# Kernel tuning notes

Measured on AMD Instinct MI355X. Metric: run time of the kernel, lower is better.

## Reference

```python
import jax, jax.numpy as jnp
import numpy as np

D = 256; H = 4; HD = 64; WBAND = 64; KLOC = 8; EMAK = 256
SUMDECAY = 0.9; STATEDECAY = 0.9; STEP = 0.5


def _dwconv(x, kern, pad):
    # x: (B,T,D), kern: (D,1,K) cross-correlation taps, causal left pad
    lhs = jnp.transpose(x, (0, 2, 1))
    out = jax.lax.conv_general_dilated(
        lhs, kern, (1,), [(pad, 0)],
        dimension_numbers=('NCH', 'OIH', 'NCH'),
        feature_group_count=x.shape[-1])
    return jnp.transpose(out, (0, 2, 1))


def _ln(x, g, b):
    m = jnp.mean(x, -1, keepdims=True)
    v = jnp.var(x, -1, keepdims=True)
    return (x - m) * jax.lax.rsqrt(v + 1e-5) * g + b


def _lin(x, w, b):
    return jnp.dot(x, w.T) + b


def _forward(parallel_repr, sequential_state, trajectory_summary, conv_w, conv_b,
             qkv_w, qkv_b, mo_w, mo_b, fg_w, fg_b, gkv_w, gkv_b, go_w, go_b,
             comb_w, comb_b, ffn1_w, ffn1_b, ffn2_w, ffn2_b, tr1_w, tr1_b,
             tr2_w, tr2_b, p2s_w, p2s_b, s2p_w, s2p_b,
             ln1_g, ln1_b, ln2_g, ln2_b, ln3_g, ln3_b, ln4_g, ln4_b):
    B, T, _ = parallel_repr.shape
    # Tier 1: local depthwise causal conv (window 8); torch pads both sides then slices [:T] == causal left pad
    local_history = _dwconv(parallel_repr, conv_w, KLOC - 1) + conv_b
    # Tier 2: banded causal attention (keep j in [i-63, i])
    qkv = _lin(parallel_repr, qkv_w, qkv_b).reshape(B, T, 3, H, HD)
    qkv = jnp.transpose(qkv, (2, 0, 3, 1, 4))  # (3,B,H,T,HD)
    q, k, v = qkv[0], qkv[1], qkv[2]
    idx = jnp.arange(T)
    band = (idx[:, None] >= idx[None, :]) & (idx[None, :] > idx[:, None] - WBAND)
    scores = jnp.einsum('bhqd,bhkd->bhqk', q, k) / jnp.sqrt(jnp.float32(HD))
    attn = jax.nn.softmax(jnp.where(band, scores, -1e9), -1)
    med = jnp.einsum('bhqk,bhkd->bhqd', attn, v)
    med = jnp.transpose(med, (0, 2, 1, 3)).reshape(B, T, D)
    med = _lin(med, mo_w, mo_b)
    fg = jax.nn.sigmoid(_lin(jnp.concatenate([parallel_repr, med], -1), fg_w, fg_b))
    medium_out = med * fg
    # Tier 3: causal cumulative (linear-attention style) global concepts
    gkv = _lin(parallel_repr, gkv_w, gkv_b)
    gk, gv = jnp.split(gkv, 2, -1)
    gk = jax.nn.elu(gk) + 1.0
    concepts = jnp.cumsum(gk * gv, 1) / (jnp.cumsum(gk, 1) + 1e-5)
    global_out = _lin(concepts, go_w, go_b)
    combined = _lin(jnp.concatenate([local_history, medium_out, global_out], -1), comb_w, comb_b)
    pr = _ln(parallel_repr + combined, ln1_g, ln1_b)
    # EMA summary via 256-tap causal depthwise conv: w[i] = (1-d)*d^i
    kE = min(T, EMAK)
    taps = (1.0 - SUMDECAY) * SUMDECAY ** jnp.arange(kE, dtype=jnp.float32)
    kern = jnp.broadcast_to(taps[::-1][None, None, :], (D, 1, kE))
    global_summary = _dwconv(pr, kern, kE - 1)
    guidance = _lin(pr, p2s_w, p2s_b)
    cs = jnp.concatenate([pr + 0.3 * guidance, global_summary], -1)
    deltas = jnp.tanh(_lin(jax.nn.gelu(_lin(cs, tr1_w, tr1_b), approximate=False), tr2_w, tr2_b))
    scaled = deltas * STEP
    # state accumulation via conv trick: acc[t] = sum_i d^i * delta[t-i]
    staps = STATEDECAY ** jnp.arange(kE, dtype=jnp.float32)
    skern = jnp.broadcast_to(staps[::-1][None, None, :], (D, 1, kE))
    acc = _dwconv(scaled, skern, kE - 1)
    dpow = STATEDECAY ** jnp.arange(1, T + 1, dtype=jnp.float32)
    pre_ln = sequential_state[:, None, :] * dpow[None, :, None] + acc
    states = _ln(pre_ln, ln3_g, ln3_b)
    seq_g = _lin(states, s2p_w, s2p_b)
    ffn = _lin(jax.nn.gelu(_lin(pr + 0.3 * seq_g, ffn1_w, ffn1_b), approximate=False), ffn2_w, ffn2_b)
    pr_out = _ln(pr + ffn, ln2_g, ln2_b)
    final_state = _ln(states[:, -1, :], ln4_g, ln4_b)
    final_traj = global_summary[:, -1, :]
    return pr_out, final_state, final_traj


def setup_inputs():
    key = jax.random.key(0)
    ks = jax.random.split(key, 20)
    B, T = 4, 2048
    s = 0.02
    def w(i, shape):
        return jax.random.normal(ks[i], shape, jnp.float32) * s
    return {
        'parallel_repr': jax.random.normal(ks[0], (B, T, D), jnp.float32),
        'sequential_state': jax.random.normal(ks[1], (B, D), jnp.float32),
        'trajectory_summary': jax.random.normal(ks[2], (B, D), jnp.float32),
        'conv_w': w(3, (D, 1, KLOC)), 'conv_b': jnp.zeros((D,)),
        'qkv_w': w(4, (3 * D, D)), 'qkv_b': jnp.zeros((3 * D,)),
        'mo_w': w(5, (D, D)), 'mo_b': jnp.zeros((D,)),
        'fg_w': w(6, (D, 2 * D)), 'fg_b': jnp.zeros((D,)),
        'gkv_w': w(7, (2 * D, D)), 'gkv_b': jnp.zeros((2 * D,)),
        'go_w': w(8, (D, D)), 'go_b': jnp.zeros((D,)),
        'comb_w': w(9, (D, 3 * D)), 'comb_b': jnp.zeros((D,)),
        'ffn1_w': w(10, (4 * D, D)), 'ffn1_b': jnp.zeros((4 * D,)),
        'ffn2_w': w(11, (D, 4 * D)), 'ffn2_b': jnp.zeros((D,)),
        'tr1_w': w(12, (2 * D, 2 * D)), 'tr1_b': jnp.zeros((2 * D,)),
        'tr2_w': w(13, (D, 2 * D)), 'tr2_b': jnp.zeros((D,)),
        'p2s_w': w(14, (D, D)), 'p2s_b': jnp.zeros((D,)),
        's2p_w': w(15, (D, D)), 's2p_b': jnp.zeros((D,)),
        'ln1_g': jnp.ones((D,)), 'ln1_b': jnp.zeros((D,)),
        'ln2_g': jnp.ones((D,)), 'ln2_b': jnp.zeros((D,)),
        'ln3_g': jnp.ones((D,)), 'ln3_b': jnp.zeros((D,)),
        'ln4_g': jnp.ones((D,)), 'ln4_b': jnp.zeros((D,)),
    }


def reference(parallel_repr, sequential_state, trajectory_summary, conv_w, conv_b,
              qkv_w, qkv_b, mo_w, mo_b, fg_w, fg_b, gkv_w, gkv_b, go_w, go_b,
              comb_w, comb_b, ffn1_w, ffn1_b, ffn2_w, ffn2_b, tr1_w, tr1_b,
              tr2_w, tr2_b, p2s_w, p2s_b, s2p_w, s2p_b,
              ln1_g, ln1_b, ln2_g, ln2_b, ln3_g, ln3_b, ln4_g, ln4_b):
    return _forward(parallel_repr, sequential_state, trajectory_summary, conv_w, conv_b,
                    qkv_w, qkv_b, mo_w, mo_b, fg_w, fg_b, gkv_w, gkv_b, go_w, go_b,
                    comb_w, comb_b, ffn1_w, ffn1_b, ffn2_w, ffn2_b, tr1_w, tr1_b,
                    tr2_w, tr2_b, p2s_w, p2s_b, s2p_w, s2p_b,
                    ln1_g, ln1_b, ln2_g, ln2_b, ln3_g, ln3_b, ln4_g, ln4_b)
```

## Files before the change

kernel.cpp:

```cpp
#include <hip/hip_runtime.h>
#include <hip/hip_bf16.h>
#include <math.h>

#define D_  256
#define T_  2048
#define B_  4
#define M_  (B_*T_)
#define H_  4
#define HD_ 64

#define NC_ 64
#define LCH (T_/NC_)

enum { OP_NONE=0, OP_SIGMUL=1, OP_ADDAUX=2, OP_AXPBY=3, OP_GELU=4, OP_TANHHALF=5 };

typedef short short8 __attribute__((ext_vector_type(8)));
typedef float f32x4  __attribute__((ext_vector_type(4)));

__device__ __forceinline__ float gelu_f(float x){ return 0.5f*x*(1.0f+erff(x*0.70710678118654752f)); }
__device__ __forceinline__ float sigmoid_f(float x){ return 1.0f/(1.0f+expf(-x)); }

__device__ __forceinline__ unsigned pk2(float a, float b){
    __hip_bfloat162 h = __float22bfloat162_rn(make_float2(a,b));
    union { __hip_bfloat162 h; unsigned u; } c; c.h = h; return c.u;
}

__global__ __launch_bounds__(256) void gemm_k(
    const float* __restrict__ A0, const float* __restrict__ W0, int ldw0, int K0,
    const float* __restrict__ A1, const float* __restrict__ W1, int ldw1, int K1,
    const float* __restrict__ A2, const float* __restrict__ W2, int ldw2, int K2,
    const float* __restrict__ bias, const float* __restrict__ aux,
    float* __restrict__ C, int ldc, int op, int ncol, float* __restrict__ vt)
{
    __shared__ unsigned short As[64*64];
    __shared__ unsigned short Ws[64*64];

    const int q8   = gridDim.x >> 3;
    const int lid  = (blockIdx.x & 7)*q8 + (blockIdx.x >> 3);
    const int brow = lid / ncol;
    const int bcol = lid - brow*ncol;
    const int row0 = brow*64, col0 = bcol*64;

    const int tid  = threadIdx.x;
    const int lane = tid & 63, wid = tid >> 6;
    const int wm = (wid >> 1)*32, wn = (wid & 1)*32;
    const int l15 = lane & 15, l4 = lane >> 4;
    const int srow = tid >> 3;
    const int sc8  = (tid & 7) * 8;

    f32x4 acc[2][2];
    #pragma unroll
    for (int i=0;i<2;++i)
        #pragma unroll
        for (int j=0;j<2;++j) acc[i][j] = (f32x4){0.f,0.f,0.f,0.f};

    float4 ra0,ra1,ra2,ra3, rw0,rw1,rw2,rw3;

    auto loadtile = [&](const float* A, const float* W, int ldw, int K, int kb){
        const float* ga = A + (size_t)(row0+srow)*K + kb + sc8;
        const float* ga2 = ga + (size_t)32*K;
        const float* gw = W + (size_t)(col0+srow)*ldw + kb + sc8;
        const float* gw2 = gw + (size_t)32*ldw;
        ra0 = *(const float4*)ga;  ra1 = *(const float4*)(ga+4);
        ra2 = *(const float4*)ga2; ra3 = *(const float4*)(ga2+4);
        rw0 = *(const float4*)gw;  rw1 = *(const float4*)(gw+4);
        rw2 = *(const float4*)gw2; rw3 = *(const float4*)(gw2+4);
    };
    auto storetile = [&](){
        const int i0 = (srow*64 + sc8) ^ ((srow&7)<<3);
        *(uint4*)&As[i0] = (uint4){pk2(ra0.x,ra0.y),pk2(ra0.z,ra0.w),pk2(ra1.x,ra1.y),pk2(ra1.z,ra1.w)};
        *(uint4*)&Ws[i0] = (uint4){pk2(rw0.x,rw0.y),pk2(rw0.z,rw0.w),pk2(rw1.x,rw1.y),pk2(rw1.z,rw1.w)};
        const int r2 = srow + 32;
        const int i1 = (r2*64 + sc8) ^ ((r2&7)<<3);
        *(uint4*)&As[i1] = (uint4){pk2(ra2.x,ra2.y),pk2(ra2.z,ra2.w),pk2(ra3.x,ra3.y),pk2(ra3.z,ra3.w)};
        *(uint4*)&Ws[i1] = (uint4){pk2(rw2.x,rw2.y),pk2(rw2.z,rw2.w),pk2(rw3.x,rw3.y),pk2(rw3.z,rw3.w)};
    };
    auto mfma_tile = [&](){
        #pragma unroll
        for (int ks=0;ks<2;++ks){
            const int koff = ks*32 + l4*8;
            short8 af[2], bf[2];
            #pragma unroll
            for (int f=0;f<2;++f){
                const int ar = wm + f*16 + l15;
                af[f] = *(const short8*)&As[(ar*64 + koff) ^ ((ar&7)<<3)];
                const int brn = wn + f*16 + l15;
                bf[f] = *(const short8*)&Ws[(brn*64 + koff) ^ ((brn&7)<<3)];
            }
            #pragma unroll
            for (int fm=0;fm<2;++fm)
                #pragma unroll
                for (int fn=0;fn<2;++fn)
                    acc[fm][fn] = __builtin_amdgcn_mfma_f32_16x16x32_bf16(
                        af[fm], bf[fn], acc[fm][fn], 0, 0, 0);
        }
    };

    const float* Ac = A0; const float* Wc = W0; int ldwc = ldw0, Kc = K0, kb = 0;
    loadtile(Ac, Wc, ldwc, Kc, 0);
    while (true){
        __syncthreads();
        storetile();
        __syncthreads();
        int nkb = kb + 64;
        const float* nA = Ac; const float* nW = Wc; int nld = ldwc, nK = Kc;
        bool have_next = true;
        if (nkb >= Kc){
            if (Ac == A0 && A1){ nA = A1; nW = W1; nld = ldw1; nK = K1; nkb = 0; }
            else if (Ac == A1 && A2){ nA = A2; nW = W2; nld = ldw2; nK = K2; nkb = 0; }
            else have_next = false;
        }
        if (have_next) loadtile(nA, nW, nld, nK, nkb);
        mfma_tile();
        if (!have_next) break;
        Ac = nA; Wc = nW; ldwc = nld; Kc = nK; kb = nkb;
    }

    #pragma unroll
    for (int fn=0;fn<2;++fn){
        const int n = col0 + wn + fn*16 + l15;
        const float bv = bias[n];
        const bool vwr = (vt != nullptr) && (n >= 512) && (n < 768);
        #pragma unroll
        for (int fm=0;fm<2;++fm){
            #pragma unroll
            for (int j=0;j<4;++j){
                const int m = row0 + wm + fm*16 + l4*4 + j;
                float v = acc[fm][fn][j] + bv;
                if (op==OP_GELU)          v = gelu_f(v);
                else if (op==OP_TANHHALF) v = 0.5f*tanhf(v);
                else if (op==OP_SIGMUL)   v = aux[(size_t)m*D_ + n]*sigmoid_f(v);
                else if (op==OP_ADDAUX)   v = v + aux[(size_t)m*D_ + n];
                else if (op==OP_AXPBY)    v = aux[(size_t)m*D_ + n] + 0.3f*v;
                C[(size_t)m*ldc + n] = v;
                if (vwr){
                    const int hh = (n-512)>>6, dd = (n-512)&63;
                    const int bb = m >> 11, tt = m & (T_-1);
                    vt[(((size_t)(bb*H_ + hh))*64 + dd)*T_ + tt] = v;
                }
            }
        }
    }
}

__global__ __launch_bounds__(256) void conv_k(const float* __restrict__ X,
    const float* __restrict__ w, const float* __restrict__ bias, float* __restrict__ out)
{
    int idx = blockIdx.x*256 + threadIdx.x;
    int d = idx & (D_-1);
    int bt = idx >> 8;
    int t = bt & (T_-1);
    float acc = bias[d];
    const float* xp = X + (size_t)bt*D_ + d;
    const float* wp = w + d*8;
    #pragma unroll
    for (int j=0;j<8;++j){
        int tt = t - 7 + j;
        if (tt >= 0) acc += xp[(size_t)(j-7)*D_] * wp[j];
    }
    out[idx] = acc;
}

__global__ __launch_bounds__(256) void attn_k(const float* __restrict__ QKVG,
    const float* __restrict__ VT, float* __restrict__ MED)
{
    __shared__ unsigned short Kl[128*64];
    __shared__ unsigned short Ql[64*64];
    __shared__ unsigned short Vl[64*128];
    const int b = blockIdx.z, h = blockIdx.y;
    const int t0 = blockIdx.x * 64;
    const int kb0 = t0 - 64;
    const int tid = threadIdx.x;

    {
        const int r0 = tid >> 3, c8 = (tid & 7) * 8;
        #pragma unroll
        for (int rep=0;rep<4;++rep){
            const int r = r0 + rep*32;
            const int kg = kb0 + r;
            uint4 pk = {0,0,0,0};
            if (kg >= 0){
                const float* gp = QKVG + ((size_t)(b*T_ + kg))*1280 + 256 + h*HD_ + c8;
                float4 x0 = *(const float4*)gp, x1 = *(const float4*)(gp+4);
                pk = (uint4){pk2(x0.x,x0.y),pk2(x0.z,x0.w),pk2(x1.x,x1.y),pk2(x1.z,x1.w)};
            }
            *(uint4*)&Kl[(r*64 + c8) ^ ((r&7)<<3)] = pk;
        }
        #pragma unroll
        for (int rep=0;rep<2;++rep){
            const int r = r0 + rep*32;
            const float* gp = QKVG + ((size_t)(b*T_ + t0 + r))*1280 + h*HD_ + c8;
            float4 x0 = *(const float4*)gp, x1 = *(const float4*)(gp+4);
            uint4 pq = (uint4){pk2(x0.x,x0.y),pk2(x0.z,x0.w),pk2(x1.x,x1.y),pk2(x1.z,x1.w)};
            *(uint4*)&Ql[(r*64 + c8) ^ ((r&7)<<3)] = pq;
        }
    }
    {
        const int d0 = tid >> 4, c8 = (tid & 15) * 8;
        #pragma unroll
        for (int rep=0;rep<4;++rep){
            const int d = d0 + rep*16;
            uint4 pv = {0,0,0,0};
            if (kb0 + c8 >= 0){
                const float* gp = VT + ((size_t)(b*H_ + h)*64 + d)*T_ + kb0 + c8;
                float4 x0 = *(const float4*)gp, x1 = *(const float4*)(gp+4);
                pv = (uint4){pk2(x0.x,x0.y),pk2(x0.z,x0.w),pk2(x1.x,x1.y),pk2(x1.z,x1.w)};
            }
            *(uint4*)&Vl[(d*128 + c8) ^ ((d&7)<<3)] = pv;
        }
    }
    __syncthreads();

    const int lane = tid & 63, w = tid >> 6;
    const int l15 = lane & 15, l4 = lane >> 4;

    short8 bq[2];
    {
        const int qr = w*16 + l15;
        bq[0] = *(const short8*)&Ql[(qr*64 +      l4*8) ^ ((qr&7)<<3)];
        bq[1] = *(const short8*)&Ql[(qr*64 + 32 + l4*8) ^ ((qr&7)<<3)];
    }

    f32x4 s[8];
    #pragma unroll
    for (int kf=0;kf<8;++kf){
        const int kr = kf*16 + l15;
        short8 a0 = *(const short8*)&Kl[(kr*64 +      l4*8) ^ ((kr&7)<<3)];
        short8 a1 = *(const short8*)&Kl[(kr*64 + 32 + l4*8) ^ ((kr&7)<<3)];
        f32x4 acc = (f32x4){0.f,0.f,0.f,0.f};
        acc = __builtin_amdgcn_mfma_f32_16x16x32_bf16(a0, bq[0], acc, 0,0,0);
        acc = __builtin_amdgcn_mfma_f32_16x16x32_bf16(a1, bq[1], acc, 0,0,0);
        s[kf] = acc;
    }

    const int qg = t0 + w*16 + l15;
    float m = -1e30f;
    #pragma unroll
    for (int kf=0;kf<8;++kf){
        #pragma unroll
        for (int j=0;j<4;++j){
            const int kg = kb0 + kf*16 + l4*4 + j;
            const int diff = qg - kg;
            const float v = (kg >= 0 && diff >= 0 && diff < 64) ? s[kf][j]*0.125f : -1e30f;
            s[kf][j] = v;
            m = fmaxf(m, v);
        }
    }
    m = fmaxf(m, __shfl_xor(m,16));
    m = fmaxf(m, __shfl_xor(m,32));
    float lsum = 0.f;
    unsigned lo[8], hi[8];
    #pragma unroll
    for (int kf=0;kf<8;++kf){
        const float p0 = expf(s[kf][0]-m), p1 = expf(s[kf][1]-m);
        const float p2 = expf(s[kf][2]-m), p3 = expf(s[kf][3]-m);
        lsum += (p0+p1)+(p2+p3);
        lo[kf] = pk2(p0,p1);
        hi[kf] = pk2(p2,p3);
    }
    lsum += __shfl_xor(lsum,16);
    lsum += __shfl_xor(lsum,32);
    const float inv = 1.f/lsum;

    f32x4 o[4];
    #pragma unroll
    for (int df=0;df<4;++df) o[df] = (f32x4){0.f,0.f,0.f,0.f};
    const int baseLane = l15 + ((l4&1)<<5);
    const bool hiHalf = (l4>>1) != 0;
    #pragma unroll
    for (int kb=0;kb<4;++kb){
        const int x0 = __shfl((int)lo[2*kb],   baseLane);
        const int x1 = __shfl((int)hi[2*kb],   baseLane);
        const int x2 = __shfl((int)lo[2*kb],   baseLane+16);
        const int x3 = __shfl((int)hi[2*kb],   baseLane+16);
        const int y0 = __shfl((int)lo[2*kb+1], baseLane);
        const int y1 = __shfl((int)hi[2*kb+1], baseLane);
        const int y2 = __shfl((int)lo[2*kb+1], baseLane+16);
        const int y3 = __shfl((int)hi[2*kb+1], baseLane+16);
        int4 afi;
        afi.x = hiHalf ? y0 : x0;
        afi.y = hiHalf ? y1 : x1;
        afi.z = hiHalf ? y2 : x2;
        afi.w = hiHalf ? y3 : x3;
        union { int4 i; short8 s; } cv; cv.i = afi;
        #pragma unroll
        for (int df=0;df<4;++df){
            const int vr = df*16 + l15;
            short8 bv = *(const short8*)&Vl[(vr*128 + kb*32 + l4*8) ^ ((vr&7)<<3)];
            o[df] = __builtin_amdgcn_mfma_f32_16x16x32_bf16(cv.s, bv, o[df], 0,0,0);
        }
    }

    #pragma unroll
    for (int j=0;j<4;++j){
        const float invj = __shfl(inv, l4*4 + j);
        const int mrow = b*T_ + t0 + w*16 + l4*4 + j;
        float* op = MED + (size_t)mrow*D_ + h*HD_ + l15;
        #pragma unroll
        for (int df=0;df<4;++df)
            op[df*16] = o[df][j] * invj;
    }
}

__global__ __launch_bounds__(256) void scan1_p1(const float* __restrict__ QKVG,
    float* __restrict__ CA, float* __restrict__ CC)
{
    const int d = threadIdx.x, c = blockIdx.x, b = blockIdx.y;
    const float* base = QKVG + ((size_t)(b*T_ + c*LCH))*1280;
    float sgk=0.f, sgkv=0.f;
    for (int t=0;t<LCH;++t){
        float gk = base[(size_t)t*1280 + 768 + d];
        gk = gk > 0.f ? gk + 1.f : expf(gk);
        float gv = base[(size_t)t*1280 + 1024 + d];
        sgk += gk; sgkv += gk*gv;
    }
    CA[((size_t)b*NC_ + c)*D_ + d] = sgk;
    CC[((size_t)b*NC_ + c)*D_ + d] = sgkv;
}

__global__ void scan1_p2(float* __restrict__ CA, float* __restrict__ CC)
{
    int idx = blockIdx.x*256 + threadIdx.x;
    int d = idx & (D_-1), b = idx >> 8;
    float sa=0.f, sc=0.f;
    for (int c=0;c<NC_;++c){
        size_t o = ((size_t)b*NC_ + c)*D_ + d;
        float a = CA[o], cc = CC[o];
        CA[o] = sa; CC[o] = sc;
        sa += a; sc += cc;
    }
}

__global__ __launch_bounds__(256) void scan1_p3(const float* __restrict__ QKVG,
    const float* __restrict__ CA, const float* __restrict__ CC, float* __restrict__ CONC)
{
    const int d = threadIdx.x, c = blockIdx.x, b = blockIdx.y;
    float sgk  = CA[((size_t)b*NC_ + c)*D_ + d];
    float sgkv = CC[((size_t)b*NC_ + c)*D_ + d];
    const float* base = QKVG + ((size_t)(b*T_ + c*LCH))*1280;
    float* out = CONC + ((size_t)(b*T_ + c*LCH))*D_ + d;
    for (int t=0;t<LCH;++t){
        float gk = base[(size_t)t*1280 + 768 + d];
        gk = gk > 0.f ? gk + 1.f : expf(gk);
        float gv = base[(size_t)t*1280 + 1024 + d];
        sgk += gk; sgkv += gk*gv;
        out[(size_t)t*D_] = sgkv / (sgk + 1e-5f);
    }
}

__global__ __launch_bounds__(256) void ema_p1(const float* __restrict__ X,
    float* __restrict__ CARRY, float alpha)
{
    const int d = threadIdx.x, c = blockIdx.x, b = blockIdx.y;
    const float* xp = X + ((size_t)(b*T_ + c*LCH))*D_ + d;
    float g = 0.f;
    for (int t=0;t<LCH;++t) g = 0.9f*g + alpha*xp[(size_t)t*D_];
    CARRY[((size_t)b*NC_ + c)*D_ + d] = g;
}

__global__ void ema_p2(float* __restrict__ CARRY, float* __restrict__ traj)
{
    int idx = blockIdx.x*256 + threadIdx.x;
    int d = idx & (D_-1), b = idx >> 8;
    const float dL = powf(0.9f, (float)LCH);
    float run = 0.f;
    for (int c=0;c<NC_;++c){
        size_t o = ((size_t)b*NC_ + c)*D_ + d;
        float loc = CARRY[o];
        CARRY[o] = run;
        run = loc + dL*run;
    }
    if (traj) traj[b*D_ + d] = run;
}

__global__ __launch_bounds__(256) void ema_p3(const float* __restrict__ X,
    const float* __restrict__ CARRY, float* __restrict__ OUT, float alpha)
{
    const int d = threadIdx.x, c = blockIdx.x, b = blockIdx.y;
    float g = CARRY[((size_t)b*NC_ + c)*D_ + d];
    const float* xp = X + ((size_t)(b*T_ + c*LCH))*D_ + d;
    float* op = OUT + ((size_t)(b*T_ + c*LCH))*D_ + d;
    for (int t=0;t<LCH;++t){
        g = 0.9f*g + alpha*xp[(size_t)t*D_];
        op[(size_t)t*D_] = g;
    }
}

__global__ __launch_bounds__(256) void ema_p3_state(const float* __restrict__ X,
    const float* __restrict__ CARRY, const float* __restrict__ SEQ, float* __restrict__ OUT)
{
    const int d = threadIdx.x, c = blockIdx.x, b = blockIdx.y;
    float a = CARRY[((size_t)b*NC_ + c)*D_ + d];
    const float ss = SEQ[b*D_ + d];
    float dp = powf(0.9f, (float)(c*LCH + 1));
    const float* xp = X + ((size_t)(b*T_ + c*LCH))*D_ + d;
    float* op = OUT + ((size_t)(b*T_ + c*LCH))*D_ + d;
    for (int t=0;t<LCH;++t){
        a = 0.9f*a + xp[(size_t)t*D_];
        op[(size_t)t*D_] = fmaf(ss, dp, a);
        dp *= 0.9f;
    }
}

__global__ __launch_bounds__(256) void ln_k(const float* __restrict__ in,
    const float* __restrict__ g, const float* __restrict__ b, float* __restrict__ out)
{
    int row  = blockIdx.x*4 + (threadIdx.x>>6);
    int lane = threadIdx.x & 63;
    const float* ip = in + (size_t)row*D_ + lane*4;
    float4 x = *(const float4*)ip;
    float s  = x.x+x.y+x.z+x.w;
    float s2 = x.x*x.x + x.y*x.y + x.z*x.z + x.w*x.w;
    #pragma unroll
    for (int o=1;o<64;o<<=1){ s += __shfl_xor(s,o); s2 += __shfl_xor(s2,o); }
    float mean = s * (1.f/256.f);
    float var  = s2 * (1.f/256.f) - mean*mean;
    float rs = rsqrtf(var + 1e-5f);
    int db = lane*4;
    float4 r;
    r.x=(x.x-mean)*rs*g[db+0]+b[db+0];
    r.y=(x.y-mean)*rs*g[db+1]+b[db+1];
    r.z=(x.z-mean)*rs*g[db+2]+b[db+2];
    r.w=(x.w-mean)*rs*g[db+3]+b[db+3];
    *(float4*)(out + (size_t)row*D_ + db) = r;
}

__global__ __launch_bounds__(256) void ln3_k(const float* __restrict__ in,
    const float* __restrict__ g3, const float* __restrict__ b3, float* __restrict__ states,
    const float* __restrict__ g4, const float* __restrict__ b4, float* __restrict__ fsout)
{
    int row  = blockIdx.x*4 + (threadIdx.x>>6);
    int lane = threadIdx.x & 63;
    const float* ip = in + (size_t)row*D_ + lane*4;
    float4 x = *(const float4*)ip;
    float s  = x.x+x.y+x.z+x.w;
    float s2 = x.x*x.x + x.y*x.y + x.z*x.z + x.w*x.w;
    #pragma unroll
    for (int o=1;o<64;o<<=1){ s += __shfl_xor(s,o); s2 += __shfl_xor(s2,o); }
    float mean = s * (1.f/256.f);
    float var  = s2 * (1.f/256.f) - mean*mean;
    float rs = rsqrtf(var + 1e-5f);
    int db = lane*4;
    float4 st;
    st.x=(x.x-mean)*rs*g3[db+0]+b3[db+0];
    st.y=(x.y-mean)*rs*g3[db+1]+b3[db+1];
    st.z=(x.z-mean)*rs*g3[db+2]+b3[db+2];
    st.w=(x.w-mean)*rs*g3[db+3]+b3[db+3];
    *(float4*)(states + (size_t)row*D_ + db) = st;

    if ((row & (T_-1)) == T_-1){
        float u  = st.x+st.y+st.z+st.w;
        float u2 = st.x*st.x + st.y*st.y + st.z*st.z + st.w*st.w;
        #pragma unroll
        for (int o=1;o<64;o<<=1){ u += __shfl_xor(u,o); u2 += __shfl_xor(u2,o); }
        float m2 = u * (1.f/256.f);
        float v2 = u2 * (1.f/256.f) - m2*m2;
        float r2 = rsqrtf(v2 + 1e-5f);
        float4 fs;
        fs.x=(st.x-m2)*r2*g4[db+0]+b4[db+0];
        fs.y=(st.y-m2)*r2*g4[db+1]+b4[db+1];
        fs.z=(st.z-m2)*r2*g4[db+2]+b4[db+2];
        fs.w=(st.w-m2)*r2*g4[db+3]+b4[db+3];
        *(float4*)(fsout + (size_t)(row>>11)*D_ + db) = fs;
    }
}

extern "C" void kernel_launch(void* const* d_in, const int* in_sizes, int n_in,
                              void* d_out, int out_size, void* d_ws, size_t ws_size,
                              hipStream_t stream)
{
    const float* X     = (const float*)d_in[0];
    const float* SEQ   = (const float*)d_in[1];
    const float* conv_w= (const float*)d_in[3];
    const float* conv_b= (const float*)d_in[4];
    const float* qkv_w = (const float*)d_in[5];
    const float* qkv_b = (const float*)d_in[6];
    const float* mo_w  = (const float*)d_in[7];
    const float* mo_b  = (const float*)d_in[8];
    const float* fg_w  = (const float*)d_in[9];
    const float* fg_b  = (const float*)d_in[10];
    const float* gkv_w = (const float*)d_in[11];
    const float* gkv_b = (const float*)d_in[12];
    const float* go_w  = (const float*)d_in[13];
    const float* go_b  = (const float*)d_in[14];
    const float* comb_w= (const float*)d_in[15];
    const float* comb_b= (const float*)d_in[16];
    const float* ffn1_w= (const float*)d_in[17];
    const float* ffn1_b= (const float*)d_in[18];
    const float* ffn2_w= (const float*)d_in[19];
    const float* ffn2_b= (const float*)d_in[20];
    const float* tr1_w = (const float*)d_in[21];
    const float* tr1_b = (const float*)d_in[22];
    const float* tr2_w = (const float*)d_in[23];
    const float* tr2_b = (const float*)d_in[24];
    const float* p2s_w = (const float*)d_in[25];
    const float* p2s_b = (const float*)d_in[26];
    const float* s2p_w = (const float*)d_in[27];
    const float* s2p_b = (const float*)d_in[28];
    const float* ln1_g = (const float*)d_in[29];
    const float* ln1_b = (const float*)d_in[30];
    const float* ln2_g = (const float*)d_in[31];
    const float* ln2_b = (const float*)d_in[32];
    const float* ln3_g = (const float*)d_in[33];
    const float* ln3_b = (const float*)d_in[34];
    const float* ln4_g = (const float*)d_in[35];
    const float* ln4_b = (const float*)d_in[36];

    float* ws   = (float*)d_ws;
    float* QKVG = ws;
    float* H1   = QKVG + (size_t)M_*1280;
    float* BUF2 = H1   + (size_t)M_*512;
    float* BUF3 = BUF2 + (size_t)M_*256;
    float* BUF4 = BUF3 + (size_t)M_*256;
    float* BUF5 = BUF4 + (size_t)M_*256;
    float* BUF6 = BUF5 + (size_t)M_*256;
    float* H2   = QKVG;
    float* VT   = BUF5;

    float* CAR0 = H1;
    float* CAR1 = H1 + (size_t)B_*NC_*D_;

    float* out_pr = (float*)d_out;
    float* out_fs = out_pr + (size_t)M_*256;
    float* out_tj = out_fs + B_*256;

    const dim3 blk256(256);
    const dim3 scan_grid(NC_, B_);
    const int NR = M_/64;

    gemm_k<<<dim3(NR*12), blk256, 0, stream>>>(
        X, qkv_w, 256, 256,  nullptr,nullptr,0,0,  nullptr,nullptr,0,0,
        qkv_b, nullptr, QKVG, 1280, OP_NONE, 12, VT);
    gemm_k<<<dim3(NR*8), blk256, 0, stream>>>(
        X, gkv_w, 256, 256,  nullptr,nullptr,0,0,  nullptr,nullptr,0,0,
        gkv_b, nullptr, QKVG+768, 1280, OP_NONE, 8, nullptr);
    conv_k<<<dim3(M_*D_/256), blk256, 0, stream>>>(X, conv_w, conv_b, BUF2);
    attn_k<<<dim3(T_/64, H_, B_), blk256, 0, stream>>>(QKVG, VT, BUF3);
    gemm_k<<<dim3(NR*4), blk256, 0, stream>>>(
        BUF3, mo_w, 256, 256,  nullptr,nullptr,0,0,  nullptr,nullptr,0,0,
        mo_b, nullptr, BUF4, 256, OP_NONE, 4, nullptr);
    scan1_p1<<<scan_grid, blk256, 0, stream>>>(QKVG, CAR0, CAR1);
    scan1_p2<<<dim3(4), blk256, 0, stream>>>(CAR0, CAR1);
    scan1_p3<<<scan_grid, blk256, 0, stream>>>(QKVG, CAR0, CAR1, BUF5);
    gemm_k<<<dim3(NR*4), blk256, 0, stream>>>(
        BUF5, go_w, 256, 256,  nullptr,nullptr,0,0,  nullptr,nullptr,0,0,
        go_b, nullptr, BUF6, 256, OP_NONE, 4, nullptr);
    gemm_k<<<dim3(NR*4), blk256, 0, stream>>>(
        X, fg_w, 512, 256,  BUF4, fg_w+256, 512, 256,  nullptr,nullptr,0,0,
        fg_b, BUF4, BUF3, 256, OP_SIGMUL, 4, nullptr);
    gemm_k<<<dim3(NR*4), blk256, 0, stream>>>(
        BUF2, comb_w, 768, 256,  BUF3, comb_w+256, 768, 256,  BUF6, comb_w+512, 768, 256,
        comb_b, X, BUF4, 256, OP_ADDAUX, 4, nullptr);
    ln_k<<<dim3(M_/4), blk256, 0, stream>>>(BUF4, ln1_g, ln1_b, BUF5);
    ema_p1<<<scan_grid, blk256, 0, stream>>>(BUF5, CAR0, 0.1f);
    ema_p2<<<dim3(4), blk256, 0, stream>>>(CAR0, out_tj);
    ema_p3<<<scan_grid, blk256, 0, stream>>>(BUF5, CAR0, BUF6, 0.1f);
    gemm_k<<<dim3(NR*4), blk256, 0, stream>>>(
        BUF5, p2s_w, 256, 256,  nullptr,nullptr,0,0,  nullptr,nullptr,0,0,
        p2s_b, BUF5, BUF2, 256, OP_AXPBY, 4, nullptr);
    gemm_k<<<dim3(NR*8), blk256, 0, stream>>>(
        BUF2, tr1_w, 512, 256,  BUF6, tr1_w+256, 512, 256,  nullptr,nullptr,0,0,
        tr1_b, nullptr, H1, 512, OP_GELU, 8, nullptr);
    gemm_k<<<dim3(NR*4), blk256, 0, stream>>>(
        H1, tr2_w, 512, 512,  nullptr,nullptr,0,0,  nullptr,nullptr,0,0,
        tr2_b, nullptr, BUF3, 256, OP_TANHHALF, 4, nullptr);
    ema_p1<<<scan_grid, blk256, 0, stream>>>(BUF3, CAR0, 1.0f);
    ema_p2<<<dim3(4), blk256, 0, stream>>>(CAR0, nullptr);
    ema_p3_state<<<scan_grid, blk256, 0, stream>>>(BUF3, CAR0, SEQ, BUF4);
    ln3_k<<<dim3(M_/4), blk256, 0, stream>>>(BUF4, ln3_g, ln3_b, BUF6, ln4_g, ln4_b, out_fs);
    gemm_k<<<dim3(NR*4), blk256, 0, stream>>>(
        BUF6, s2p_w, 256, 256,  nullptr,nullptr,0,0,  nullptr,nullptr,0,0,
        s2p_b, BUF5, BUF2, 256, OP_AXPBY, 4, nullptr);
    gemm_k<<<dim3(NR*16), blk256, 0, stream>>>(
        BUF2, ffn1_w, 256, 256,  nullptr,nullptr,0,0,  nullptr,nullptr,0,0,
        ffn1_b, nullptr, H2, 1024, OP_GELU, 16, nullptr);
    gemm_k<<<dim3(NR*4), blk256, 0, stream>>>(
        H2, ffn2_w, 1024, 1024,  nullptr,nullptr,0,0,  nullptr,nullptr,0,0,
        ffn2_b, BUF5, BUF3, 256, OP_ADDAUX, 4, nullptr);
    ln_k<<<dim3(M_/4), blk256, 0, stream>>>(BUF3, ln2_g, ln2_b, out_pr);
}
```

Baseline: 275.2 us.

## Store intermediate activations and weights in bf16 and merge QKV/GKV GEMMs

Adds a conversion kernel that casts all weights and the input to bf16 once per call, then changes the GEMMs, attention, scan and EMA kernels to read and write bf16 intermediates instead of fp32. The aim is to roughly halve global memory traffic and to drop the per-tile fp32-to-bf16 packing inside the GEMM loaders. It also fuses the separate QKV and GKV projections into one 1280-column GEMM. In exchange it adds a conversion pass over about 1.8M weight elements and the input on every call, and rounds more intermediates (including V, attention output and concepts) to bf16, which reduces precision.

After: 255.8 us. 1.08x faster.

```diff
diff --git a/kernel.cpp b/kernel.cpp
--- a/kernel.cpp
+++ b/kernel.cpp
@@ -14,6 +14,7 @@
 
 enum { OP_NONE=0, OP_SIGMUL=1, OP_ADDAUX=2, OP_AXPBY=3, OP_GELU=4, OP_TANHHALF=5 };
 
+typedef unsigned short u16;
 typedef short short8 __attribute__((ext_vector_type(8)));
 typedef float f32x4  __attribute__((ext_vector_type(4)));
 
@@ -24,16 +25,73 @@
     __hip_bfloat162 h = __float22bfloat162_rn(make_float2(a,b));
     union { __hip_bfloat162 h; unsigned u; } c; c.h = h; return c.u;
 }
+__device__ __forceinline__ float bfu(u16 u){ return __uint_as_float(((unsigned)u)<<16); }
+__device__ __forceinline__ u16 bf1(float x){ return (u16)(pk2(x,x)&0xffffu); }
+
+#define OFF_QKV   0u
+#define OFF_MO    327680u
+#define OFF_FG    393216u
+#define OFF_GO    524288u
+#define OFF_COMB  589824u
+#define OFF_FFN1  786432u
+#define OFF_FFN2  1048576u
+#define OFF_TR1   1310720u
+#define OFF_TR2   1572864u
+#define OFF_P2S   1703936u
+#define OFF_S2P   1769472u
+#define NWELEM    1835008u
+#define NXELEM    2097152u
+
+__global__ __launch_bounds__(256) void cvt_k(
+    const float* __restrict__ qkv_w, const float* __restrict__ gkv_w,
+    const float* __restrict__ qkv_b, const float* __restrict__ gkv_b,
+    const float* __restrict__ mo_w,  const float* __restrict__ fg_w,
+    const float* __restrict__ go_w,  const float* __restrict__ comb_w,
+    const float* __restrict__ ffn1_w,const float* __restrict__ ffn2_w,
+    const float* __restrict__ tr1_w, const float* __restrict__ tr2_w,
+    const float* __restrict__ p2s_w, const float* __restrict__ s2p_w,
+    const float* __restrict__ X,
+    u16* __restrict__ Wh, u16* __restrict__ Xh, float* __restrict__ bq)
+{
+    size_t i = ((size_t)blockIdx.x*256 + threadIdx.x)*4;
+    if (i < NWELEM){
+        const float* s; size_t base;
+        if      (i < OFF_MO)  { s=(i<196608)?qkv_w:gkv_w; base=(i<196608)?0:196608; }
+        else if (i < OFF_FG)  { s=mo_w;   base=OFF_MO; }
+        else if (i < OFF_GO)  { s=fg_w;   base=OFF_FG; }
+        else if (i < OFF_COMB){ s=go_w;   base=OFF_GO; }
+        else if (i < OFF_FFN1){ s=comb_w; base=OFF_COMB; }
+        else if (i < OFF_FFN2){ s=ffn1_w; base=OFF_FFN1; }
+        else if (i < OFF_TR1) { s=ffn2_w; base=OFF_FFN2; }
+        else if (i < OFF_TR2) { s=tr1_w;  base=OFF_TR1; }
+        else if (i < OFF_P2S) { s=tr2_w;  base=OFF_TR2; }
+        else if (i < OFF_S2P) { s=p2s_w;  base=OFF_P2S; }
+        else                  { s=s2p_w;  base=OFF_S2P; }
+        float4 v = *(const float4*)(s + (i-base));
+        *(uint2*)(Wh + i) = (uint2){ pk2(v.x,v.y), pk2(v.z,v.w) };
+    } else if (i < NWELEM + NXELEM){
+        size_t j = i - NWELEM;
+        float4 v = *(const float4*)(X + j);
+        *(uint2*)(Xh + j) = (uint2){ pk2(v.x,v.y), pk2(v.z,v.w) };
+    } else if (i < NWELEM + NXELEM + 1280){
+        size_t j = i - (NWELEM + NXELEM);
+        #pragma unroll
+        for (int k=0;k<4;++k){
+            size_t e = j + k;
+            bq[e] = (e < 768) ? qkv_b[e] : gkv_b[e-768];
+        }
+    }
+}
 
 __global__ __launch_bounds__(256) void gemm_k(
-    const float* __restrict__ A0, const float* __restrict__ W0, int ldw0, int K0,
-    const float* __restrict__ A1, const float* __restrict__ W1, int ldw1, int K1,
-    const float* __restrict__ A2, const float* __restrict__ W2, int ldw2, int K2,
-    const float* __restrict__ bias, const float* __restrict__ aux,
-    float* __restrict__ C, int ldc, int op, int ncol, float* __restrict__ vt)
-{
-    __shared__ unsigned short As[64*64];
-    __shared__ unsigned short Ws[64*64];
+    const u16* __restrict__ A0, const u16* __restrict__ W0, int ldw0, int K0,
+    const u16* __restrict__ A1, const u16* __restrict__ W1, int ldw1, int K1,
+    const u16* __restrict__ A2, const u16* __restrict__ W2, int ldw2, int K2,
+    const float* __restrict__ bias, const void* __restrict__ aux, int aux_bf16,
+    void* __restrict__ C, int ldc, int c_bf16, int op, int ncol, u16* __restrict__ vt)
+{
+    __shared__ u16 As[64*64];
+    __shared__ u16 Ws[64*64];
 
     const int q8   = gridDim.x >> 3;
     const int lid  = (blockIdx.x & 7)*q8 + (blockIdx.x >> 3);
@@ -54,26 +112,22 @@
         #pragma unroll
         for (int j=0;j<2;++j) acc[i][j] = (f32x4){0.f,0.f,0.f,0.f};
 
-    float4 ra0,ra1,ra2,ra3, rw0,rw1,rw2,rw3;
-
-    auto loadtile = [&](const float* A, const float* W, int ldw, int K, int kb){
-        const float* ga = A + (size_t)(row0+srow)*K + kb + sc8;
-        const float* ga2 = ga + (size_t)32*K;
-        const float* gw = W + (size_t)(col0+srow)*ldw + kb + sc8;
-        const float* gw2 = gw + (size_t)32*ldw;
-        ra0 = *(const float4*)ga;  ra1 = *(const float4*)(ga+4);
-        ra2 = *(const float4*)ga2; ra3 = *(const float4*)(ga2+4);
-        rw0 = *(const float4*)gw;  rw1 = *(const float4*)(gw+4);
-        rw2 = *(const float4*)gw2; rw3 = *(const float4*)(gw2+4);
+    uint4 ra0, ra1, rw0, rw1;
+
+    auto loadtile = [&](const u16* A, const u16* W, int ldw, int K, int kb){
+        const u16* ga = A + (size_t)(row0+srow)*K + kb + sc8;
+        ra0 = *(const uint4*)ga;
+        ra1 = *(const uint4*)(ga + (size_t)32*K);
+        const u16* gw = W + (size_t)(col0+srow)*ldw + kb + sc8;
+        rw0 = *(const uint4*)gw;
+        rw1 = *(const uint4*)(gw + (size_t)32*ldw);
     };
     auto storetile = [&](){
         const int i0 = (srow*64 + sc8) ^ ((srow&7)<<3);
-        *(uint4*)&As[i0] = (uint4){pk2(ra0.x,ra0.y),pk2(ra0.z,ra0.w),pk2(ra1.x,ra1.y),pk2(ra1.z,ra1.w)};
-        *(uint4*)&Ws[i0] = (uint4){pk2(rw0.x,rw0.y),pk2(rw0.z,rw0.w),pk2(rw1.x,rw1.y),pk2(rw1.z,rw1.w)};
+        *(uint4*)&As[i0] = ra0;  *(uint4*)&Ws[i0] = rw0;
         const int r2 = srow + 32;
         const int i1 = (r2*64 + sc8) ^ ((r2&7)<<3);
-        *(uint4*)&As[i1] = (uint4){pk2(ra2.x,ra2.y),pk2(ra2.z,ra2.w),pk2(ra3.x,ra3.y),pk2(ra3.z,ra3.w)};
-        *(uint4*)&Ws[i1] = (uint4){pk2(rw2.x,rw2.y),pk2(rw2.z,rw2.w),pk2(rw3.x,rw3.y),pk2(rw3.z,rw3.w)};
+        *(uint4*)&As[i1] = ra1;  *(uint4*)&Ws[i1] = rw1;
     };
     auto mfma_tile = [&](){
         #pragma unroll
@@ -96,14 +150,14 @@
         }
     };
 
-    const float* Ac = A0; const float* Wc = W0; int ldwc = ldw0, Kc = K0, kb = 0;
+    const u16* Ac = A0; const u16* Wc = W0; int ldwc = ldw0, Kc = K0, kb = 0;
     loadtile(Ac, Wc, ldwc, Kc, 0);
     while (true){
         __syncthreads();
         storetile();
         __syncthreads();
         int nkb = kb + 64;
-        const float* nA = Ac; const float* nW = Wc; int nld = ldwc, nK = Kc;
+        const u16* nA = Ac; const u16* nW = Wc; int nld = ldwc, nK = Kc;
         bool have_next = true;
         if (nkb >= Kc){
             if (Ac == A0 && A1){ nA = A1; nW = W1; nld = ldw1; nK = K1; nkb = 0; }
@@ -129,14 +183,20 @@
                 float v = acc[fm][fn][j] + bv;
                 if (op==OP_GELU)          v = gelu_f(v);
                 else if (op==OP_TANHHALF) v = 0.5f*tanhf(v);
-                else if (op==OP_SIGMUL)   v = aux[(size_t)m*D_ + n]*sigmoid_f(v);
-                else if (op==OP_ADDAUX)   v = v + aux[(size_t)m*D_ + n];
-                else if (op==OP_AXPBY)    v = aux[(size_t)m*D_ + n] + 0.3f*v;
-                C[(size_t)m*ldc + n] = v;
+                else if (op!=OP_NONE){
+                    const size_t ai = (size_t)m*D_ + n;
+                    const float a = aux_bf16 ? bfu(((const u16*)aux)[ai])
+                                             : ((const float*)aux)[ai];
+                    if (op==OP_SIGMUL)      v = a*sigmoid_f(v);
+                    else if (op==OP_ADDAUX) v = v + a;
+                    else                    v = a + 0.3f*v;
+                }
+                if (c_bf16) ((u16*)C)[(size_t)m*ldc + n] = bf1(v);
+                else        ((float*)C)[(size_t)m*ldc + n] = v;
                 if (vwr){
                     const int hh = (n-512)>>6, dd = (n-512)&63;
                     const int bb = m >> 11, tt = m & (T_-1);
-                    vt[(((size_t)(bb*H_ + hh))*64 + dd)*T_ + tt] = v;
+                    vt[(((size_t)(bb*H_ + hh))*64 + dd)*T_ + tt] = bf1(v);
                 }
             }
         }
@@ -144,7 +204,7 @@
 }
 
 __global__ __launch_bounds__(256) void conv_k(const float* __restrict__ X,
-    const float* __restrict__ w, const float* __restrict__ bias, float* __restrict__ out)
+    const float* __restrict__ w, const float* __restrict__ bias, u16* __restrict__ out)
 {
     int idx = blockIdx.x*256 + threadIdx.x;
     int d = idx & (D_-1);
@@ -158,15 +218,15 @@
         int tt = t - 7 + j;
         if (tt >= 0) acc += xp[(size_t)(j-7)*D_] * wp[j];
     }
-    out[idx] = acc;
-}
-
-__global__ __launch_bounds__(256) void attn_k(const float* __restrict__ QKVG,
-    const float* __restrict__ VT, float* __restrict__ MED)
-{
-    __shared__ unsigned short Kl[128*64];
-    __shared__ unsigned short Ql[64*64];
-    __shared__ unsigned short Vl[64*128];
+    out[idx] = bf1(acc);
+}
+
+__global__ __launch_bounds__(256) void attn_k(const u16* __restrict__ QKVG,
+    const u16* __restrict__ VT, u16* __restrict__ MED)
+{
+    __shared__ u16 Kl[128*64];
+    __shared__ u16 Ql[64*64];
+    __shared__ u16 Vl[64*128];
     const int b = blockIdx.z, h = blockIdx.y;
     const int t0 = blockIdx.x * 64;
     const int kb0 = t0 - 64;
@@ -179,19 +239,14 @@
             const int r = r0 + rep*32;
             const int kg = kb0 + r;
             uint4 pk = {0,0,0,0};
-            if (kg >= 0){
-                const float* gp = QKVG + ((size_t)(b*T_ + kg))*1280 + 256 + h*HD_ + c8;
-                float4 x0 = *(const float4*)gp, x1 = *(const float4*)(gp+4);
-                pk = (uint4){pk2(x0.x,x0.y),pk2(x0.z,x0.w),pk2(x1.x,x1.y),pk2(x1.z,x1.w)};
-            }
+            if (kg >= 0)
+                pk = *(const uint4*)(QKVG + ((size_t)(b*T_ + kg))*1280 + 256 + h*HD_ + c8);
             *(uint4*)&Kl[(r*64 + c8) ^ ((r&7)<<3)] = pk;
         }
         #pragma unroll
         for (int rep=0;rep<2;++rep){
             const int r = r0 + rep*32;
-            const float* gp = QKVG + ((size_t)(b*T_ + t0 + r))*1280 + h*HD_ + c8;
-            float4 x0 = *(const float4*)gp, x1 = *(const float4*)(gp+4);
-            uint4 pq = (uint4){pk2(x0.x,x0.y),pk2(x0.z,x0.w),pk2(x1.x,x1.y),pk2(x1.z,x1.w)};
+            uint4 pq = *(const uint4*)(QKVG + ((size_t)(b*T_ + t0 + r))*1280 + h*HD_ + c8);
             *(uint4*)&Ql[(r*64 + c8) ^ ((r&7)<<3)] = pq;
         }
     }
@@ -201,11 +256,8 @@
         for (int rep=0;rep<4;++rep){
             const int d = d0 + rep*16;
             uint4 pv = {0,0,0,0};
-            if (kb0 + c8 >= 0){
-                const float* gp = VT + ((size_t)(b*H_ + h)*64 + d)*T_ + kb0 + c8;
-                float4 x0 = *(const float4*)gp, x1 = *(const float4*)(gp+4);
-                pv = (uint4){pk2(x0.x,x0.y),pk2(x0.z,x0.w),pk2(x1.x,x1.y),pk2(x1.z,x1.w)};
-            }
+            if (kb0 + c8 >= 0)
+                pv = *(const uint4*)(VT + ((size_t)((b*H_ + h)*64 + d))*T_ + kb0 + c8);
             *(uint4*)&Vl[(d*128 + c8) ^ ((d&7)<<3)] = pv;
         }
     }
@@ -295,23 +347,23 @@
     for (int j=0;j<4;++j){
         const float invj = __shfl(inv, l4*4 + j);
         const int mrow = b*T_ + t0 + w*16 + l4*4 + j;
-        float* op = MED + (size_t)mrow*D_ + h*HD_ + l15;
+        u16* op = MED + (size_t)mrow*D_ + h*HD_ + l15;
         #pragma unroll
         for (int df=0;df<4;++df)
-            op[df*16] = o[df][j] * invj;
-    }
-}
-
-__global__ __launch_bounds__(256) void scan1_p1(const float* __restrict__ QKVG,
+            op[df*16] = bf1(o[df][j] * invj);
+    }
+}
+
+__global__ __launch_bounds__(256) void scan1_p1(const u16* __restrict__ QKVG,
     float* __restrict__ CA, float* __restrict__ CC)
 {
     const int d = threadIdx.x, c = blockIdx.x, b = blockIdx.y;
-    const float* base = QKVG + ((size_t)(b*T_ + c*LCH))*1280;
+    const u16* base = QKVG + ((size_t)(b*T_ + c*LCH))*1280;
     float sgk=0.f, sgkv=0.f;
     for (int t=0;t<LCH;++t){
-        float gk = base[(size_t)t*1280 + 768 + d];
+        float gk = bfu(base[(size_t)t*1280 + 768 + d]);
         gk = gk > 0.f ? gk + 1.f : expf(gk);
-        float gv = base[(size_t)t*1280 + 1024 + d];
+        float gv = bfu(base[(size_t)t*1280 + 1024 + d]);
         sgk += gk; sgkv += gk*gv;
     }
     CA[((size_t)b*NC_ + c)*D_ + d] = sgk;
@@ -331,20 +383,20 @@
     }
 }
 
-__global__ __launch_bounds__(256) void scan1_p3(const float* __restrict__ QKVG,
-    const float* __restrict__ CA, const float* __restrict__ CC, float* __restrict__ CONC)
+__global__ __launch_bounds__(256) void scan1_p3(const u16* __restrict__ QKVG,
+    const float* __restrict__ CA, const float* __restrict__ CC, u16* __restrict__ CONC)
 {
     const int d = threadIdx.x, c = blockIdx.x, b = blockIdx.y;
     float sgk  = CA[((size_t)b*NC_ + c)*D_ + d];
     float sgkv = CC[((size_t)b*NC_ + c)*D_ + d];
-    const float* base = QKVG + ((size_t)(b*T_ + c*LCH))*1280;
-    float* out = CONC + ((size_t)(b*T_ + c*LCH))*D_ + d;
+    const u16* base = QKVG + ((size_t)(b*T_ + c*LCH))*1280;
+    u16* out = CONC + ((size_t)(b*T_ + c*LCH))*D_ + d;
     for (int t=0;t<LCH;++t){
-        float gk = base[(size_t)t*1280 + 768 + d];
+        float gk = bfu(base[(size_t)t*1280 + 768 + d]);
         gk = gk > 0.f ? gk + 1.f : expf(gk);
-        float gv = base[(size_t)t*1280 + 1024 + d];
+        float gv = bfu(base[(size_t)t*1280 + 1024 + d]);
         sgk += gk; sgkv += gk*gv;
-        out[(size_t)t*D_] = sgkv / (sgk + 1e-5f);
+        out[(size_t)t*D_] = bf1(sgkv / (sgk + 1e-5f));
     }
 }
 
@@ -373,16 +425,16 @@
     if (traj) traj[b*D_ + d] = run;
 }
 
-__global__ __launch_bounds__(256) void ema_p3(const float* __restrict__ X,
-    const float* __restrict__ CARRY, float* __restrict__ OUT, float alpha)
+__global__ __launch_bounds__(256) void ema_p3h(const float* __restrict__ X,
+    const float* __restrict__ CARRY, u16* __restrict__ OUT, float alpha)
 {
     const int d = threadIdx.x, c = blockIdx.x, b = blockIdx.y;
     float g = CARRY[((size_t)b*NC_ + c)*D_ + d];
     const float* xp = X + ((size_t)(b*T_ + c*LCH))*D_ + d;
-    float* op = OUT + ((size_t)(b*T_ + c*LCH))*D_ + d;
+    u16* op = OUT + ((size_t)(b*T_ + c*LCH))*D_ + d;
     for (int t=0;t<LCH;++t){
         g = 0.9f*g + alpha*xp[(size_t)t*D_];
-        op[(size_t)t*D_] = g;
+        op[(size_t)t*D_] = bf1(g);
     }
 }
 
@@ -403,7 +455,8 @@
 }
 
 __global__ __launch_bounds__(256) void ln_k(const float* __restrict__ in,
-    const float* __restrict__ g, const float* __restrict__ b, float* __restrict__ out)
+    const float* __restrict__ g, const float* __restrict__ b,
+    float* __restrict__ out, u16* __restrict__ out2)
 {
     int row  = blockIdx.x*4 + (threadIdx.x>>6);
     int lane = threadIdx.x & 63;
@@ -423,10 +476,12 @@
     r.z=(x.z-mean)*rs*g[db+2]+b[db+2];
     r.w=(x.w-mean)*rs*g[db+3]+b[db+3];
     *(float4*)(out + (size_t)row*D_ + db) = r;
+    if (out2)
+        *(uint2*)(out2 + (size_t)row*D_ + db) = (uint2){ pk2(r.x,r.y), pk2(r.z,r.w) };
 }
 
 __global__ __launch_bounds__(256) void ln3_k(const float* __restrict__ in,
-    const float* __restrict__ g3, const float* __restrict__ b3, float* __restrict__ states,
+    const float* __restrict__ g3, const float* __restrict__ b3, u16* __restrict__ states,
     const float* __restrict__ g4, const float* __restrict__ b4, float* __restrict__ fsout)
 {
     int row  = blockIdx.x*4 + (threadIdx.x>>6);
@@ -446,7 +501,7 @@
     st.y=(x.y-mean)*rs*g3[db+1]+b3[db+1];
     st.z=(x.z-mean)*rs*g3[db+2]+b3[db+2];
     st.w=(x.w-mean)*rs*g3[db+3]+b3[db+3];
-    *(float4*)(states + (size_t)row*D_ + db) = st;
+    *(uint2*)(states + (size_t)row*D_ + db) = (uint2){ pk2(st.x,st.y), pk2(st.z,st.w) };
 
     if ((row & (T_-1)) == T_-1){
         float u  = st.x+st.y+st.z+st.w;
@@ -506,19 +561,34 @@
     const float* ln4_g = (const float*)d_in[35];
     const float* ln4_b = (const float*)d_in[36];
 
-    float* ws   = (float*)d_ws;
-    float* QKVG = ws;
-    float* H1   = QKVG + (size_t)M_*1280;
-    float* BUF2 = H1   + (size_t)M_*512;
-    float* BUF3 = BUF2 + (size_t)M_*256;
-    float* BUF4 = BUF3 + (size_t)M_*256;
-    float* BUF5 = BUF4 + (size_t)M_*256;
-    float* BUF6 = BUF5 + (size_t)M_*256;
-    float* H2   = QKVG;
-    float* VT   = BUF5;
-
-    float* CAR0 = H1;
-    float* CAR1 = H1 + (size_t)B_*NC_*D_;
+    char* p = (char*)d_ws;
+    auto alloc = [&](size_t bytes)->char*{ char* r = p; p += (bytes + 255) & ~(size_t)255; return r; };
+
+    u16*   QKVG = (u16*)  alloc((size_t)M_*1280*2);
+    u16*   Wh   = (u16*)  alloc((size_t)NWELEM*2);
+    float* bq   = (float*)alloc(1280*4);
+    u16*   Xh   = (u16*)  alloc((size_t)M_*256*2);
+    u16*   VTh  = (u16*)  alloc((size_t)M_*256*2);
+    u16*   MED  = (u16*)  alloc((size_t)M_*256*2);
+    u16*   MED2 = (u16*)  alloc((size_t)M_*256*2);
+    u16*   LH   = (u16*)  alloc((size_t)M_*256*2);
+    u16*   CONC = (u16*)  alloc((size_t)M_*256*2);
+    u16*   GOUT = (u16*)  alloc((size_t)M_*256*2);
+    u16*   MOUT = (u16*)  alloc((size_t)M_*256*2);
+    float* PRE1 = (float*)alloc((size_t)M_*256*4);
+    float* PR   = (float*)alloc((size_t)M_*256*4);
+    u16*   PRh  = (u16*)  alloc((size_t)M_*256*2);
+    u16*   GSUM = (u16*)  alloc((size_t)M_*256*2);
+    u16*   CS1  = (u16*)  alloc((size_t)M_*256*2);
+    u16*   H1   = (u16*)  alloc((size_t)M_*512*2);
+    float* SCALED=(float*)alloc((size_t)M_*256*4);
+    float* PRE3 = (float*)alloc((size_t)M_*256*4);
+    u16*   STATESh=(u16*) alloc((size_t)M_*256*2);
+    u16*   FFNIN= (u16*)  alloc((size_t)M_*256*2);
+    u16*   H2   = (u16*)  alloc((size_t)M_*1024*2);
+    float* PRE2 = (float*)alloc((size_t)M_*256*4);
+    float* CAR0 = (float*)alloc((size_t)B_*NC_*D_*4);
+    float* CAR1 = (float*)alloc((size_t)B_*NC_*D_*4);
 
     float* out_pr = (float*)d_out;
     float* out_fs = out_pr + (size_t)M_*256;
@@ -528,54 +598,54 @@
     const dim3 scan_grid(NC_, B_);
     const int NR = M_/64;
 
-    gemm_k<<<dim3(NR*12), blk256, 0, stream>>>(
-        X, qkv_w, 256, 256,  nullptr,nullptr,0,0,  nullptr,nullptr,0,0,
-        qkv_b, nullptr, QKVG, 1280, OP_NONE, 12, VT);
-    gemm_k<<<dim3(NR*8), blk256, 0, stream>>>(
-        X, gkv_w, 256, 256,  nullptr,nullptr,0,0,  nullptr,nullptr,0,0,
-        gkv_b, nullptr, QKVG+768, 1280, OP_NONE, 8, nullptr);
-    conv_k<<<dim3(M_*D_/256), blk256, 0, stream>>>(X, conv_w, conv_b, BUF2);
-    attn_k<<<dim3(T_/64, H_, B_), blk256, 0, stream>>>(QKVG, VT, BUF3);
-    gemm_k<<<dim3(NR*4), blk256, 0, stream>>>(
-        BUF3, mo_w, 256, 256,  nullptr,nullptr,0,0,  nullptr,nullptr,0,0,
-        mo_b, nullptr, BUF4, 256, OP_NONE, 4, nullptr);
+    cvt_k<<<dim3(3842), blk256, 0, stream>>>(
+        qkv_w, gkv_w, qkv_b, gkv_b, mo_w, fg_w, go_w, comb_w,
+        ffn1_w, ffn2_w, tr1_w, tr2_w, p2s_w, s2p_w, X, Wh, Xh, bq);
+    gemm_k<<<dim3(NR*20), blk256, 0, stream>>>(
+        Xh, Wh+OFF_QKV, 256, 256,  nullptr,nullptr,0,0,  nullptr,nullptr,0,0,
+        bq, nullptr, 0, QKVG, 1280, 1, OP_NONE, 20, VTh);
+    conv_k<<<dim3(M_*D_/256), blk256, 0, stream>>>(X, conv_w, conv_b, LH);
+    attn_k<<<dim3(T_/64, H_, B_), blk256, 0, stream>>>(QKVG, VTh, MED);
+    gemm_k<<<dim3(NR*4), blk256, 0, stream>>>(
+        MED, Wh+OFF_MO, 256, 256,  nullptr,nullptr,0,0,  nullptr,nullptr,0,0,
+        mo_b, nullptr, 0, MED2, 256, 1, OP_NONE, 4, nullptr);
     scan1_p1<<<scan_grid, blk256, 0, stream>>>(QKVG, CAR0, CAR1);
     scan1_p2<<<dim3(4), blk256, 0, stream>>>(CAR0, CAR1);
-    scan1_p3<<<scan_grid, blk256, 0, stream>>>(QKVG, CAR0, CAR1, BUF5);
-    gemm_k<<<dim3(NR*4), blk256, 0, stream>>>(
-        BUF5, go_w, 256, 256,  nullptr,nullptr,0,0,  nullptr,nullptr,0,0,
-        go_b, nullptr, BUF6, 256, OP_NONE, 4, nullptr);
-    gemm_k<<<dim3(NR*4), blk256, 0, stream>>>(
-        X, fg_w, 512, 256,  BUF4, fg_w+256, 512, 256,  nullptr,nullptr,0,0,
-        fg_b, BUF4, BUF3, 256, OP_SIGMUL, 4, nullptr);
-    gemm_k<<<dim3(NR*4), blk256, 0, stream>>>(
-        BUF2, comb_w, 768, 256,  BUF3, comb_w+256, 768, 256,  BUF6, comb_w+512, 768, 256,
-        comb_b, X, BUF4, 256, OP_ADDAUX, 4, nullptr);
-    ln_k<<<dim3(M_/4), blk256, 0, stream>>>(BUF4, ln1_g, ln1_b, BUF5);
-    ema_p1<<<scan_grid, blk256, 0, stream>>>(BUF5, CAR0, 0.1f);
+    scan1_p3<<<scan_grid, blk256, 0, stream>>>(QKVG, CAR0, CAR1, CONC);
+    gemm_k<<<dim3(NR*4), blk256, 0, stream>>>(
+        CONC, Wh+OFF_GO, 256, 256,  nullptr,nullptr,0,0,  nullptr,nullptr,0,0,
+        go_b, nullptr, 0, GOUT, 256, 1, OP_NONE, 4, nullptr);
+    gemm_k<<<dim3(NR*4), blk256, 0, stream>>>(
+        Xh, Wh+OFF_FG, 512, 256,  MED2, Wh+OFF_FG+256, 512, 256,  nullptr,nullptr,0,0,
+        fg_b, MED2, 1, MOUT, 256, 1, OP_SIGMUL, 4, nullptr);
+    gemm_k<<<dim3(NR*4), blk256, 0, stream>>>(
+        LH, Wh+OFF_COMB, 768, 256,  MOUT, Wh+OFF_COMB+256, 768, 256,  GOUT, Wh+OFF_COMB+512, 768, 256,
+        comb_b, X, 0, PRE1, 256, 0, OP_ADDAUX, 4, nullptr);
+    ln_k<<<dim3(M_/4), blk256, 0, stream>>>(PRE1, ln1_g, ln1_b, PR, PRh);
+    ema_p1<<<scan_grid, blk256, 0, stream>>>(PR, CAR0, 0.1f);
     ema_p2<<<dim3(4), blk256, 0, stream>>>(CAR0, out_tj);
-    ema_p3<<<scan_grid, blk256, 0, stream>>>(BUF5, CAR0, BUF6, 0.1f);
-    gemm_k<<<dim3(NR*4), blk256, 0, stream>>>(
-        BUF5, p2s_w, 256, 256,  nullptr,nullptr,0,0,  nullptr,nullptr,0,0,
-        p2s_b, BUF5, BUF2, 256, OP_AXPBY, 4, nullptr);
+    ema_p3h<<<scan_grid, blk256, 0, stream>>>(PR, CAR0, GSUM, 0.1f);
+    gemm_k<<<dim3(NR*4), blk256, 0, stream>>>(
+        PRh, Wh+OFF_P2S, 256, 256,  nullptr,nullptr,0,0,  nullptr,nullptr,0,0,
+        p2s_b, PR, 0, CS1, 256, 1, OP_AXPBY, 4, nullptr);
     gemm_k<<<dim3(NR*8), blk256, 0, stream>>>(
-        BUF2, tr1_w, 512, 256,  BUF6, tr1_w+256, 512, 256,  nullptr,nullptr,0,0,
-        tr1_b, nullptr, H1, 512, OP_GELU, 8, nullptr);
-    gemm_k<<<dim3(NR*4), blk256, 0, stream>>>(
-        H1, tr2_w, 512, 512,  nullptr,nullptr,0,0,  nullptr,nullptr,0,0,
-        tr2_b, nullptr, BUF3, 256, OP_TANHHALF, 4, nullptr);
-    ema_p1<<<scan_grid, blk256, 0, stream>>>(BUF3, CAR0, 1.0f);
+        CS1, Wh+OFF_TR1, 512, 256,  GSUM, Wh+OFF_TR1+256, 512, 256,  nullptr,nullptr,0,0,
+        tr1_b, nullptr, 0, H1, 512, 1, OP_GELU, 8, nullptr);
+    gemm_k<<<dim3(NR*4), blk256, 0, stream>>>(
+        H1, Wh+OFF_TR2, 512, 512,  nullptr,nullptr,0,0,  nullptr,nullptr,0,0,
+        tr2_b, nullptr, 0, SCALED, 256, 0, OP_TANHHALF, 4, nullptr);
+    ema_p1<<<scan_grid, blk256, 0, stream>>>(SCALED, CAR0, 1.0f);
     ema_p2<<<dim3(4), blk256, 0, stream>>>(CAR0, nullptr);
-    ema_p3_state<<<scan_grid, blk256, 0, stream>>>(BUF3, CAR0, SEQ, BUF4);
-    ln3_k<<<dim3(M_/4), blk256, 0, stream>>>(BUF4, ln3_g, ln3_b, BUF6, ln4_g, ln4_b, out_fs);
-    gemm_k<<<dim3(NR*4), blk256, 0, stream>>>(
-        BUF6, s2p_w, 256, 256,  nullptr,nullptr,0,0,  nullptr,nullptr,0,0,
-        s2p_b, BUF5, BUF2, 256, OP_AXPBY, 4, nullptr);
+    ema_p3_state<<<scan_grid, blk256, 0, stream>>>(SCALED, CAR0, SEQ, PRE3);
+    ln3_k<<<dim3(M_/4), blk256, 0, stream>>>(PRE3, ln3_g, ln3_b, STATESh, ln4_g, ln4_b, out_fs);
+    gemm_k<<<dim3(NR*4), blk256, 0, stream>>>(
+        STATESh, Wh+OFF_S2P, 256, 256,  nullptr,nullptr,0,0,  nullptr,nullptr,0,0,
+        s2p_b, PR, 0, FFNIN, 256, 1, OP_AXPBY, 4, nullptr);
     gemm_k<<<dim3(NR*16), blk256, 0, stream>>>(
-        BUF2, ffn1_w, 256, 256,  nullptr,nullptr,0,0,  nullptr,nullptr,0,0,
-        ffn1_b, nullptr, H2, 1024, OP_GELU, 16, nullptr);
-    gemm_k<<<dim3(NR*4), blk256, 0, stream>>>(
-        H2, ffn2_w, 1024, 1024,  nullptr,nullptr,0,0,  nullptr,nullptr,0,0,
-        ffn2_b, BUF5, BUF3, 256, OP_ADDAUX, 4, nullptr);
-    ln_k<<<dim3(M_/4), blk256, 0, stream>>>(BUF3, ln2_g, ln2_b, out_pr);
-}
+        FFNIN, Wh+OFF_FFN1, 256, 256,  nullptr,nullptr,0,0,  nullptr,nullptr,0,0,
+        ffn1_b, nullptr, 0, H2, 1024, 1, OP_GELU, 16, nullptr);
+    gemm_k<<<dim3(NR*4), blk256, 0, stream>>>(
+        H2, Wh+OFF_FFN2, 1024, 1024,  nullptr,nullptr,0,0,  nullptr,nullptr,0,0,
+        ffn2_b, PR, 0, PRE2, 256, 0, OP_ADDAUX, 4, nullptr);
+    ln_k<<<dim3(M_/4), blk256, 0, stream>>>(PRE2, ln2_g, ln2_b, out_pr, nullptr);
+}
```
